# Kernel optimization log

Hardware: AMD Instinct MI355X
Metric: run time of the kernel (lower is better)

The kernel has to match this reference:

```python
import jax, jax.numpy as jnp
import numpy as np

H = 16  # head_num


def setup_inputs() -> dict:
    key = jax.random.key(0)
    ks = jax.random.split(key, 16)
    B, N, D, DR = 4, 512, 1024, 128
    dk = D // H
    nrm = lambda i, shp, sc=1.0: jax.random.normal(ks[i], shp, jnp.float32) * sc
    inp = {
        "q": nrm(0, (B, N, D)),
        "k": nrm(1, (B, N, D)),
        "v": nrm(2, (B, N, D)),
        "r_k": nrm(3, (B, N, N, DR), 0.1),
        "r_v": nrm(4, (B, N, N, DR), 0.1),
        # learned params (Linear stored as [in, out] so y = x @ W + b)
        "Wq": nrm(5, (D, D), 1.0 / np.sqrt(D)), "bq": jnp.zeros((D,), jnp.float32),
        "Wk": nrm(6, (D, D), 1.0 / np.sqrt(D)), "bk": jnp.zeros((D,), jnp.float32),
        "Wv": nrm(7, (D, D), 1.0 / np.sqrt(D)), "bv": jnp.zeros((D,), jnp.float32),
        "Wrk": nrm(8, (DR, dk), 1.0 / np.sqrt(DR)), "brk": jnp.zeros((dk,), jnp.float32),
        "Wrv": nrm(9, (DR, dk), 1.0 / np.sqrt(DR)), "brv": jnp.zeros((dk,), jnp.float32),
        "Wo": nrm(10, (D, D), 1.0 / np.sqrt(D)), "bo": jnp.zeros((D,), jnp.float32),
    }
    return inp


def reference(q, k, v, r_k, r_v, Wq, bq, Wk, bk, Wv, bv, Wrk, brk, Wrv, brv, Wo, bo):
    B, N, D = q.shape
    dk = D // H
    scale = 1.0 / np.sqrt(dk).astype(np.float32)
    # relation projections ('concat' mode, rel_share=False): [B,N,N,d_rel] -> [B,N,N,d_k]
    rk = r_k @ Wrk + brk
    rv = r_v @ Wrv + brv

    def heads(x, W, b):  # [B,N,D] -> [B,H,N,dk]
        return (x @ W + b).reshape(B, N, H, dk).transpose(0, 2, 1, 3)

    qh = heads(q, Wq, bq)
    kh = heads(k, Wk, bk)
    vh = heads(v, Wv, bv)
    # score_1: standard scaled dot-product; score_2: relation bias per (query m, key n)
    score = jnp.einsum('bhmd,bhnd->bhmn', qh, kh) * scale \
          + jnp.einsum('bhmd,bmnd->bhmn', qh, rk)
    att = jax.nn.softmax(score, axis=-1)  # [B,H,N,N]
    # value_1: standard AV; value_2: relation-value combination
    val = jnp.einsum('bhmn,bhnd->bhmd', att, vh) \
        + jnp.einsum('bhmn,bmnd->bhmd', att, rv)
    out = val.transpose(0, 2, 1, 3).reshape(B, N, D) @ Wo + bo
    return out
```

## Files before the change

kernel.cpp:

```cpp
#include <hip/hip_runtime.h>
#include <hip/hip_bf16.h>
#include <hip/hip_fp16.h>
#include <stdint.h>


typedef __attribute__((ext_vector_type(4))) float f32x4;
typedef __attribute__((ext_vector_type(8))) short s16x8;

#define MFMA16(A, B, C) __builtin_amdgcn_mfma_f32_16x16x32_bf16(A, B, C, 0, 0, 0)

__device__ __forceinline__ uint16_t f2bf(float x) {
  uint32_t u = __float_as_uint(x);
  u += 0x7fffu + ((u >> 16) & 1u);
  return (uint16_t)(u >> 16);
}
__device__ __forceinline__ float bf2f(uint16_t u) {
  return __uint_as_float((uint32_t)u << 16);
}
__device__ __forceinline__ uint16_t f2h(float x) {
  __half h = __float2half_rn(x);
  return *reinterpret_cast<uint16_t*>(&h);
}
__device__ __forceinline__ float h2f(uint16_t u) {
  __half h = *reinterpret_cast<__half*>(&u);
  return __half2float(h);
}

__device__ __forceinline__ uint32_t cvtpk(float lo, float hi) {
  uint32_t r;
  asm("v_cvt_pk_bf16_f32 %0, %1, %2" : "=v"(r) : "v"(lo), "v"(hi));
  return r;
}

__device__ __forceinline__ s16x8 pack8(float4 a, float4 b) {
  union { uint32_t u[4]; s16x8 v; } r;
  r.u[0] = cvtpk(a.x, a.y);
  r.u[1] = cvtpk(a.z, a.w);
  r.u[2] = cvtpk(b.x, b.y);
  r.u[3] = cvtpk(b.z, b.w);
  return r.v;
}

__device__ __forceinline__ void gll16(const void* g, void* l) {
  __builtin_amdgcn_global_load_lds(
      (const __attribute__((address_space(1))) uint32_t*)(g),
      (__attribute__((address_space(3))) uint32_t*)(l), 16, 0, 0);
}

__global__ __launch_bounds__(256) void k_prep(
    const float* __restrict__ Wq, const float* __restrict__ Wk,
    const float* __restrict__ Wv, const float* __restrict__ Wo,
    const float* __restrict__ Wrk, const float* __restrict__ Wrv,
    uint16_t* __restrict__ WqT, uint16_t* __restrict__ WkT,
    uint16_t* __restrict__ WvT, uint16_t* __restrict__ WoT,
    uint16_t* __restrict__ WrkB, uint16_t* __restrict__ WrvT) {
  int z = blockIdx.y;
  int t = threadIdx.x;
  if (z == 4) {
    if (blockIdx.x == 0) {
      for (int i = t; i < 128 * 64; i += 256) WrkB[i] = f2bf(Wrk[i]);
      for (int i = t; i < 64 * 128; i += 256) {
        int d = i >> 7, r = i & 127;
        WrvT[i] = f2bf(Wrv[r * 64 + d]);
      }
    }
    return;
  }
  const float* W = (z == 0) ? Wq : (z == 1) ? Wk : (z == 2) ? Wv : Wo;
  uint16_t* O = (z == 0) ? WqT : (z == 1) ? WkT : (z == 2) ? WvT : WoT;
  int tk = (blockIdx.x >> 4) * 64;
  int tn = (blockIdx.x & 15) * 64;
  __shared__ float tile[64][65];
  {
    int kk = t >> 2, c0 = (t & 3) * 16;
    const float* src = W + (size_t)(tk + kk) * 1024 + tn + c0;
#pragma unroll
    for (int i = 0; i < 16; i += 4) {
      float4 v = *(const float4*)(src + i);
      tile[kk][c0 + i + 0] = v.x; tile[kk][c0 + i + 1] = v.y;
      tile[kk][c0 + i + 2] = v.z; tile[kk][c0 + i + 3] = v.w;
    }
  }
  __syncthreads();
  {
    int n_loc = t >> 2;
    int n = tn + n_loc;
#pragma unroll
    for (int cc = 0; cc < 2; ++cc) {
      int c = (t & 3) * 2 + cc;
      int csrc = c ^ (n & 7);
      s16x8 pk;
#pragma unroll
      for (int j = 0; j < 8; ++j) pk[j] = (short)f2bf(tile[csrc * 8 + j][n_loc]);
      *reinterpret_cast<s16x8*>(O + (size_t)n * 1024 + tk + c * 8) = pk;
    }
  }
}

__global__ __launch_bounds__(256) void k_projqkv(
    const float* __restrict__ Xq, const float* __restrict__ Xk,
    const float* __restrict__ Xv, const uint16_t* __restrict__ WTbase,
    const float* __restrict__ bq, const float* __restrict__ bk,
    const float* __restrict__ bv, uint16_t* __restrict__ outbase) {
  int mode = blockIdx.z;
  const float* X = (mode == 0) ? Xq : (mode == 1) ? Xk : Xv;
  const float* bias = (mode == 0) ? bq : (mode == 1) ? bk : bv;
  const uint16_t* WT = WTbase + (size_t)mode * (1u << 20);
  uint16_t* out = outbase + (size_t)mode * (2u << 20);

  __shared__ alignas(16) float Xs[128 * 64];
  __shared__ alignas(16) uint16_t Bs[128 * 64];
  int t = threadIdx.x, lane = t & 63, w = t >> 6, lr = lane & 15, lg = lane >> 4;
  int m0 = blockIdx.x * 128, n0 = blockIdx.y * 128;
  int wm = (w >> 1) * 64, wn = (w & 1) * 64;
  f32x4 acc[4][4];
#pragma unroll
  for (int i = 0; i < 4; ++i)
#pragma unroll
    for (int j = 0; j < 4; ++j) acc[i][j] = (f32x4){0.f, 0.f, 0.f, 0.f};
  for (int ko = 0; ko < 16; ++ko) {
    __syncthreads();
    {
#pragma unroll
      for (int i = 0; i < 8; ++i) {
        int u = i * 256 + t;
        int row = u >> 4, c16 = u & 15;
        int cs = c16 ^ (row & 15);
        gll16(X + (size_t)(m0 + row) * 1024 + ko * 64 + cs * 4, (char*)Xs + u * 16);
      }
#pragma unroll
      for (int i = 0; i < 4; ++i) {
        int u = i * 256 + t;
        int row = u >> 3, c2 = u & 7;
        gll16(WT + (size_t)(n0 + row) * 1024 + ko * 64 + c2 * 8, (char*)Bs + u * 16);
      }
    }
    __syncthreads();
#pragma unroll
    for (int kk = 0; kk < 2; ++kk) {
      s16x8 af[4], bf[4];
#pragma unroll
      for (int mt = 0; mt < 4; ++mt) {
        int row = wm + mt * 16 + lr;
        int c0 = kk * 8 + lg * 2;
        float4 v0 = *(const float4*)((const char*)Xs + row * 256 +
                                     ((c0 ^ (row & 15)) * 16));
        float4 v1 = *(const float4*)((const char*)Xs + row * 256 +
                                     (((c0 + 1) ^ (row & 15)) * 16));
        af[mt] = pack8(v0, v1);
      }
#pragma unroll
      for (int nt = 0; nt < 4; ++nt) {
        int row = wn + nt * 16 + lr;
        bf[nt] = *(const s16x8*)((const char*)Bs + row * 128 +
                                 (((kk * 32 + lg * 8) * 2) ^ ((row & 7) << 4)));
      }
#pragma unroll
      for (int mt = 0; mt < 4; ++mt)
#pragma unroll
        for (int nt = 0; nt < 4; ++nt)
          acc[mt][nt] = MFMA16(af[mt], bf[nt], acc[mt][nt]);
    }
  }
  float sc = (mode == 1) ? 0.125f : 1.0f;
#pragma unroll
  for (int mt = 0; mt < 4; ++mt) {
#pragma unroll
    for (int nt = 0; nt < 4; ++nt) {
      int col = n0 + wn + nt * 16 + lr;
      float bcol = bias[col];
      if (mode != 2) {
#pragma unroll
        for (int r = 0; r < 4; ++r) {
          int row = m0 + wm + mt * 16 + lg * 4 + r;
          out[(size_t)row * 1024 + col] = f2bf((acc[mt][nt][r] + bcol) * sc);
        }
      } else {
        int row0 = m0 + wm + mt * 16 + lg * 4;
        int b = row0 >> 9, n = row0 & 511;
        int h = col >> 6, d = col & 63;
        ushort4 pk;
        pk.x = f2bf(acc[mt][nt][0] + bcol);
        pk.y = f2bf(acc[mt][nt][1] + bcol);
        pk.z = f2bf(acc[mt][nt][2] + bcol);
        pk.w = f2bf(acc[mt][nt][3] + bcol);
        *reinterpret_cast<ushort4*>(out + ((size_t)(b * 16 + h) * 64 + d) * 512 + n) = pk;
      }
    }
  }
}

__global__ __launch_bounds__(256) void k_score1qt(
    const uint16_t* __restrict__ qh, const uint16_t* __restrict__ kh,
    const uint16_t* __restrict__ WrkB, uint16_t* __restrict__ S1,
    uint16_t* __restrict__ qt) {
  __shared__ alignas(16) uint16_t As[128 * 64];
  __shared__ alignas(16) uint16_t Bs[128 * 64];
  int t = threadIdx.x, lane = t & 63, w = t >> 6, lr = lane & 15, lg = lane >> 4;
  int b = blockIdx.z;
  if (blockIdx.y >= 16) {
    int slot = (blockIdx.y - 16) * 64 + b * 16 + blockIdx.x;
#pragma unroll
    for (int it = 0; it < 2; ++it) {
      int row0 = slot * 128 + it * 64 + w * 16;
      f32x4 acc[8];
#pragma unroll
      for (int i = 0; i < 8; ++i) acc[i] = (f32x4){0.f, 0.f, 0.f, 0.f};
      s16x8 af[2];
#pragma unroll
      for (int kk = 0; kk < 2; ++kk)
        af[kk] = *(const s16x8*)(qh + (size_t)(row0 + lr) * 64 + kk * 32 + lg * 8);
#pragma unroll
      for (int rt = 0; rt < 8; ++rt) {
#pragma unroll
        for (int kk = 0; kk < 2; ++kk) {
          s16x8 bf = *(const s16x8*)(WrkB + (size_t)(rt * 16 + lr) * 64 + kk * 32 + lg * 8);
          acc[rt] = MFMA16(af[kk], bf, acc[rt]);
        }
      }
#pragma unroll
      for (int rt = 0; rt < 8; ++rt)
#pragma unroll
        for (int r = 0; r < 4; ++r)
          qt[(size_t)(row0 + lg * 4 + r) * 128 + rt * 16 + lr] = f2bf(acc[rt][r]);
    }
    return;
  }
  int mt = blockIdx.x >> 2, nt = blockIdx.x & 3, h = blockIdx.y;
  int m0 = mt * 128, n0 = nt * 128;
  const char* qg = (const char*)(qh + (size_t)(b * 512 + m0) * 1024 + h * 64);
  const char* kg = (const char*)(kh + (size_t)(b * 512 + n0) * 1024 + h * 64);
#pragma unroll
  for (int i = 0; i < 4; ++i) {
    int u = i * 256 + t;
    int row = u >> 3;
    int cs = (u & 7) ^ (row & 7);
    gll16(qg + (size_t)row * 2048 + cs * 16, (char*)As + u * 16);
    gll16(kg + (size_t)row * 2048 + cs * 16, (char*)Bs + u * 16);
  }
  __syncthreads();
  int wm = (w >> 1) * 64, wn = (w & 1) * 64;
  f32x4 acc[4][4];
#pragma unroll
  for (int i = 0; i < 4; ++i)
#pragma unroll
    for (int j = 0; j < 4; ++j) acc[i][j] = (f32x4){0.f, 0.f, 0.f, 0.f};
#pragma unroll
  for (int kk = 0; kk < 2; ++kk) {
    s16x8 af[4], bf[4];
#pragma unroll
    for (int mtt = 0; mtt < 4; ++mtt) {
      int row = wm + mtt * 16 + lr;
      af[mtt] = *(const s16x8*)((const char*)As + row * 128 +
                                (((kk * 4 + lg) ^ (row & 7)) * 16));
    }
#pragma unroll
    for (int ntt = 0; ntt < 4; ++ntt) {
      int row = wn + ntt * 16 + lr;
      bf[ntt] = *(const s16x8*)((const char*)Bs + row * 128 +
                                (((kk * 4 + lg) ^ (row & 7)) * 16));
    }
#pragma unroll
    for (int mtt = 0; mtt < 4; ++mtt)
#pragma unroll
      for (int ntt = 0; ntt < 4; ++ntt)
        acc[mtt][ntt] = MFMA16(bf[ntt], af[mtt], acc[mtt][ntt]);
  }
  int hsw = (h & 7) << 3;
#pragma unroll
  for (int mtt = 0; mtt < 4; ++mtt) {
#pragma unroll
    for (int ntt = 0; ntt < 4; ++ntt) {
      int m = b * 512 + m0 + wm + mtt * 16 + lr;
      int nsw = (n0 + wn + ntt * 16 + lg * 4) ^ hsw;
      ushort4 u4;
      u4.x = f2h(acc[mtt][ntt][0]); u4.y = f2h(acc[mtt][ntt][1]);
      u4.z = f2h(acc[mtt][ntt][2]); u4.w = f2h(acc[mtt][ntt][3]);
      *(ushort4*)(S1 + (size_t)m * 8192 + h * 512 + nsw) = u4;
    }
  }
}

#define RKSTEP(s)                                                              \
  {                                                                            \
    asm volatile("s_waitcnt vmcnt(%0)" ::                                      \
                 "i"(((s) < 2) ? 6 : (((s) < 31) ? 2 : 0)) : "memory");        \
    const char* bp_ = wpriv + ((s) & 1) * 2048 + lr * 128;                     \
    float4 v0_ = *(const float4*)(bp_ + (((lg * 2 + 0) ^ (lr & 7)) * 16));     \
    float4 v1_ = *(const float4*)(bp_ + (((lg * 2 + 1) ^ (lr & 7)) * 16));     \
    acc[(s) >> 2] = MFMA16(aqt[(s) & 3], pack8(v0_, v1_), acc[(s) >> 2]);      \
    if ((s) + 2 < 32) {                                                        \
      const int s2_ = (s) + 2;                                                 \
      const char* src_ = rkb + (size_t)((s2_ >> 2) * 64 + w * 16 + r_lo) * 512 \
                         + (s2_ & 3) * 128 + c16s * 16;                        \
      char* dst_ = wpriv + (s2_ & 1) * 2048 + lane * 16;                       \
      gll16(src_, dst_);                                                       \
      gll16(src_ + 8 * 512, dst_ + 1024);                                      \
    }                                                                          \
  }

#define RVI(c)                                                                 \
  { _Pragma("unroll")                                                          \
    for (int i_ = 0; i_ < 2; ++i_) {                                           \
      int u_ = i_ * 64 + lane;                                                 \
      gll16(rvb + (size_t)(((c) >> 1) * 32 + (u_ >> 2)) * 512 + w * 128 +      \
                ((c) & 1) * 64 + (u_ & 3) * 16,                                \
            wpriv + ((c) & 1) * 2048 + u_ * 16);                               \
    } }

#define RVC(c, accv)                                                           \
  {                                                                            \
    s16x8 a_ = *(const s16x8*)((const char*)att_lds + lr * 1024 +              \
        (((uint32_t)(((c) >> 1) * 64 + lg * 16)) ^ ((uint32_t)(lr & 7) << 4)));\
    const float* vb_ = (const float*)(wpriv + ((c) & 1) * 2048);               \
    union { uint32_t u[4]; s16x8 v; } bb_;                                     \
    _Pragma("unroll")                                                          \
    for (int i = 0; i < 4; ++i)                                                \
      bb_.u[i] = cvtpk(vb_[(lg * 8 + 2 * i) * 16 + lr],                        \
                       vb_[(lg * 8 + 2 * i + 1) * 16 + lr]);                   \
    accv = MFMA16(a_, bb_.v, accv);                                            \
  }

__global__ __launch_bounds__(256, 4) void k_s2v2(
    const uint16_t* __restrict__ qt, const float* __restrict__ rk,
    const float* __restrict__ rv, uint16_t* SATT,
    const uint16_t* __restrict__ WrvT, const float* __restrict__ brv,
    uint16_t* __restrict__ V2) {
  int bm = blockIdx.x;
  int t = threadIdx.x, lane = t & 63, w = t >> 6, lr = lane & 15, lg = lane >> 4;
  __shared__ alignas(16) char stream_lds[16384];
  __shared__ alignas(16) uint16_t att_lds[16 * 512];
  __shared__ alignas(16) uint16_t arv_lds[16 * 128];
  __shared__ float red[2][16][4];
  char* wpriv = stream_lds + w * 4096;
  const int r_lo = lane >> 3;
  const int c16s = (lane & 7) ^ r_lo;

  s16x8 aqt[4];
#pragma unroll
  for (int kk = 0; kk < 4; ++kk)
    aqt[kk] = *(const s16x8*)(qt + ((size_t)bm * 16 + lr) * 128 + kk * 32 + lg * 8);

  const char* rkb = (const char*)(rk + (size_t)bm * 65536);
#pragma unroll
  for (int s2 = 0; s2 < 2; ++s2) {
    const char* src_ = rkb + (size_t)(w * 16 + r_lo) * 512 + s2 * 128 + c16s * 16;
    char* dst_ = wpriv + s2 * 2048 + lane * 16;
    gll16(src_, dst_);
    gll16(src_ + 8 * 512, dst_ + 1024);
  }
  const char* s1g = (const char*)(SATT + (size_t)bm * 8192);
#pragma unroll
  for (int i = 0; i < 4; ++i)
    gll16(s1g + i * 4096 + t * 16, (char*)att_lds + i * 4096 + t * 16);

  f32x4 acc[8];
#pragma unroll
  for (int j = 0; j < 8; ++j) acc[j] = (f32x4){0.f, 0.f, 0.f, 0.f};

  RKSTEP(0)  RKSTEP(1)  RKSTEP(2)  RKSTEP(3)  RKSTEP(4)  RKSTEP(5)  RKSTEP(6)  RKSTEP(7)
  RKSTEP(8)  RKSTEP(9)  RKSTEP(10) RKSTEP(11) RKSTEP(12) RKSTEP(13) RKSTEP(14) RKSTEP(15)
  RKSTEP(16) RKSTEP(17) RKSTEP(18) RKSTEP(19) RKSTEP(20) RKSTEP(21) RKSTEP(22) RKSTEP(23)
  RKSTEP(24) RKSTEP(25) RKSTEP(26) RKSTEP(27) RKSTEP(28) RKSTEP(29) RKSTEP(30) RKSTEP(31)

  __syncthreads();

  const char* rvb = (const char*)(rv + (size_t)bm * 65536);
  RVI(0) RVI(1)

#pragma unroll
  for (int idx = 0; idx < 8; ++idx) {
#pragma unroll
    for (int r = 0; r < 4; ++r) {
      int h = lg * 4 + r;
      int n = idx * 64 + w * 16 + lr;
      uint16_t s1v = *(const uint16_t*)((const char*)att_lds + h * 1024 +
                     (((uint32_t)n * 2) ^ ((uint32_t)(h & 7) << 4)));
      acc[idx][r] += h2f(s1v);
    }
  }

  float mrow[4], inv[4];
#pragma unroll
  for (int r = 0; r < 4; ++r) {
    float mx = acc[0][r];
#pragma unroll
    for (int j = 1; j < 8; ++j) mx = fmaxf(mx, acc[j][r]);
#pragma unroll
    for (int off = 1; off < 16; off <<= 1) mx = fmaxf(mx, __shfl_xor(mx, off, 64));
    mrow[r] = mx;
  }
  if (lr == 0) {
#pragma unroll
    for (int r = 0; r < 4; ++r) red[0][lg * 4 + r][w] = mrow[r];
  }
  __syncthreads();
#pragma unroll
  for (int r = 0; r < 4; ++r) {
    const float* p = red[0][lg * 4 + r];
    mrow[r] = fmaxf(fmaxf(p[0], p[1]), fmaxf(p[2], p[3]));
  }
#pragma unroll
  for (int r = 0; r < 4; ++r) {
    float s = 0.f;
#pragma unroll
    for (int j = 0; j < 8; ++j) {
      float pj = __expf(acc[j][r] - mrow[r]);
      acc[j][r] = pj;
      s += pj;
    }
#pragma unroll
    for (int off = 1; off < 16; off <<= 1) s += __shfl_xor(s, off, 64);
    inv[r] = s;
  }
  if (lr == 0) {
#pragma unroll
    for (int r = 0; r < 4; ++r) red[1][lg * 4 + r][w] = inv[r];
  }
  __syncthreads();
#pragma unroll
  for (int r = 0; r < 4; ++r) {
    const float* p = red[1][lg * 4 + r];
    inv[r] = 1.f / (p[0] + p[1] + p[2] + p[3]);
  }
#pragma unroll
  for (int r = 0; r < 4; ++r) {
    int h = lg * 4 + r;
#pragma unroll
    for (int idx = 0; idx < 8; ++idx) {
      int n = idx * 64 + w * 16 + lr;
      uint32_t off = (uint32_t)h * 1024 + (((uint32_t)n * 2) ^ ((uint32_t)(h & 7) << 4));
      *(uint16_t*)((char*)att_lds + off) = f2bf(acc[idx][r] * inv[r]);
    }
  }
  __syncthreads();

  f32x4 arv0 = (f32x4){0.f, 0.f, 0.f, 0.f}, arv1 = arv0;
#pragma unroll 1
  for (int cp = 0; cp < 14; ++cp) {
    asm volatile("s_waitcnt vmcnt(2)" ::: "memory");
    RVC(2 * cp, arv0)
    RVI(2 * cp + 2)
    asm volatile("s_waitcnt vmcnt(2)" ::: "memory");
    RVC(2 * cp + 1, arv1)
    RVI(2 * cp + 3)
  }
  asm volatile("s_waitcnt vmcnt(2)" ::: "memory");
  RVC(28, arv0)
  RVI(30)
  asm volatile("s_waitcnt vmcnt(2)" ::: "memory");
  RVC(29, arv1)
  RVI(31)
  asm volatile("s_waitcnt vmcnt(2)" ::: "memory");
  RVC(30, arv0)
  asm volatile("s_waitcnt vmcnt(0)" ::: "memory");
  RVC(31, arv1)

#pragma unroll
  for (int r = 0; r < 4; ++r) {
    int h = lg * 4 + r;
    uint32_t rc0 = (uint32_t)(w * 32 + lr) * 2;
    uint32_t rc1 = (uint32_t)(w * 32 + 16 + lr) * 2;
    *(uint16_t*)((char*)arv_lds + h * 256 + (rc0 ^ ((uint32_t)(h & 7) << 4))) = f2bf(arv0[r]);
    *(uint16_t*)((char*)arv_lds + h * 256 + (rc1 ^ ((uint32_t)(h & 7) << 4))) = f2bf(arv1[r]);
  }
  __syncthreads();
  f32x4 vacc = (f32x4){0.f, 0.f, 0.f, 0.f};
#pragma unroll
  for (int kk = 0; kk < 4; ++kk) {
    uint32_t rb = (uint32_t)(kk * 32 + lg * 8) * 2;
    s16x8 a = *(const s16x8*)((const char*)arv_lds + lr * 256 +
                              (rb ^ ((uint32_t)(lr & 7) << 4)));
    s16x8 bfw = *(const s16x8*)(WrvT + (size_t)(w * 16 + lr) * 128 + kk * 32 + lg * 8);
    vacc = MFMA16(a, bfw, vacc);
  }
  float bias = brv[w * 16 + lr];
#pragma unroll
  for (int r = 0; r < 4; ++r)
    V2[(size_t)bm * 1024 + (lg * 4 + r) * 64 + w * 16 + lr] = f2bf(vacc[r] + bias);

#pragma unroll
  for (int i = 0; i < 4; ++i) {
    s16x8 vv = *(const s16x8*)((const char*)att_lds + i * 4096 + t * 16);
    *(s16x8*)((char*)SATT + (size_t)bm * 16384 + i * 4096 + t * 16) = vv;
  }
}

__global__ __launch_bounds__(256, 4) void k_val1(
    const uint16_t* __restrict__ vhT, const uint16_t* __restrict__ ATT,
    const uint16_t* __restrict__ V2, uint16_t* __restrict__ VALB) {
  int t = threadIdx.x, lane = t & 63, w = t >> 6, lr = lane & 15, lg = lane >> 4;
  int mt = blockIdx.x >> 1, dh = blockIdx.x & 1, h = blockIdx.y, b = blockIdx.z;
  int mb = mt * 64 + w * 16;
  const uint16_t* vrow = vhT + ((size_t)((b * 16 + h) * 64) + dh * 32 + lr) * 512 + lg * 8;
  const uint16_t* arow = ATT + (size_t)(b * 512 + mb + lr) * 8192 + h * 512;
  f32x4 acc[2];
#pragma unroll
  for (int j = 0; j < 2; ++j) acc[j] = (f32x4){0.f, 0.f, 0.f, 0.f};
#pragma unroll
  for (int kk = 0; kk < 16; ++kk) {
    int nsw = (kk * 32 + lg * 8) ^ ((h & 7) << 3);
    s16x8 a0 = *(const s16x8*)(arow + nsw);
#pragma unroll
    for (int dt = 0; dt < 2; ++dt) {
      s16x8 vf = *(const s16x8*)(vrow + (size_t)dt * 16 * 512 + kk * 32);
      acc[dt] = MFMA16(vf, a0, acc[dt]);
    }
  }
#pragma unroll
  for (int dt = 0; dt < 2; ++dt) {
    size_t adr = (size_t)(b * 512 + mb + lr) * 1024 + h * 64 + dh * 32 + dt * 16 + lg * 4;
    ushort4 v2v = *(const ushort4*)(V2 + adr);
    ushort4 o;
    o.x = f2bf(acc[dt][0] + bf2f(v2v.x));
    o.y = f2bf(acc[dt][1] + bf2f(v2v.y));
    o.z = f2bf(acc[dt][2] + bf2f(v2v.z));
    o.w = f2bf(acc[dt][3] + bf2f(v2v.w));
    *(ushort4*)(VALB + adr) = o;
  }
}

__global__ __launch_bounds__(256) void k_out(
    const uint16_t* __restrict__ A, const uint16_t* __restrict__ WT,
    const float* __restrict__ bias, float* __restrict__ out) {
  __shared__ alignas(16) uint16_t As[128 * 64];
  __shared__ alignas(16) uint16_t Bs[128 * 64];
  int t = threadIdx.x, lane = t & 63, w = t >> 6, lr = lane & 15, lg = lane >> 4;
  int m0 = blockIdx.x * 128, n0 = blockIdx.y * 128;
  int wm = (w >> 1) * 64, wn = (w & 1) * 64;
  f32x4 acc[4][4];
#pragma unroll
  for (int i = 0; i < 4; ++i)
#pragma unroll
    for (int j = 0; j < 4; ++j) acc[i][j] = (f32x4){0.f, 0.f, 0.f, 0.f};
  for (int ko = 0; ko < 16; ++ko) {
    __syncthreads();
    {
#pragma unroll
      for (int i = 0; i < 4; ++i) {
        int u = i * 256 + t;
        int row = u >> 3, c2 = u & 7;
        int cs = c2 ^ (row & 7);
        gll16(A + (size_t)(m0 + row) * 1024 + ko * 64 + cs * 8, (char*)As + u * 16);
        gll16(WT + (size_t)(n0 + row) * 1024 + ko * 64 + c2 * 8, (char*)Bs + u * 16);
      }
    }
    __syncthreads();
#pragma unroll
    for (int kk = 0; kk < 2; ++kk) {
      s16x8 af[4], bf[4];
#pragma unroll
      for (int mt = 0; mt < 4; ++mt) {
        int row = wm + mt * 16 + lr;
        af[mt] = *(const s16x8*)((const char*)As + row * 128 +
                                 (((kk * 32 + lg * 8) * 2) ^ ((row & 7) << 4)));
      }
#pragma unroll
      for (int nt = 0; nt < 4; ++nt) {
        int row = wn + nt * 16 + lr;
        bf[nt] = *(const s16x8*)((const char*)Bs + row * 128 +
                                 (((kk * 32 + lg * 8) * 2) ^ ((row & 7) << 4)));
      }
#pragma unroll
      for (int mt = 0; mt < 4; ++mt)
#pragma unroll
        for (int nt = 0; nt < 4; ++nt)
          acc[mt][nt] = MFMA16(af[mt], bf[nt], acc[mt][nt]);
    }
  }
#pragma unroll
  for (int mt = 0; mt < 4; ++mt) {
#pragma unroll
    for (int nt = 0; nt < 4; ++nt) {
      int col = n0 + wn + nt * 16 + lr;
      float bcol = bias[col];
#pragma unroll
      for (int r = 0; r < 4; ++r) {
        int row = m0 + wm + mt * 16 + lg * 4 + r;
        out[(size_t)row * 1024 + col] = acc[mt][nt][r] + bcol;
      }
    }
  }
}

extern "C" void kernel_launch(void* const* d_in, const int* in_sizes, int n_in,
                              void* d_out, int out_size, void* d_ws, size_t ws_size,
                              hipStream_t stream) {
  const float* q   = (const float*)d_in[0];
  const float* k_  = (const float*)d_in[1];
  const float* v   = (const float*)d_in[2];
  const float* r_k = (const float*)d_in[3];
  const float* r_v = (const float*)d_in[4];
  const float* Wq  = (const float*)d_in[5];
  const float* bq  = (const float*)d_in[6];
  const float* Wk  = (const float*)d_in[7];
  const float* bk  = (const float*)d_in[8];
  const float* Wv  = (const float*)d_in[9];
  const float* bv  = (const float*)d_in[10];
  const float* Wrk = (const float*)d_in[11];
  const float* Wrv = (const float*)d_in[13];
  const float* brv = (const float*)d_in[14];
  const float* Wo  = (const float*)d_in[15];
  const float* bo  = (const float*)d_in[16];
  (void)in_sizes; (void)n_in; (void)out_size;

  char* ws = (char*)d_ws;
  uint16_t* WqT  = (uint16_t*)(ws + (size_t)(0));
  uint16_t* WkT  = (uint16_t*)(ws + (size_t)(2u << 20));
  uint16_t* WvT  = (uint16_t*)(ws + (size_t)(4u << 20));
  uint16_t* WoT  = (uint16_t*)(ws + (size_t)(6u << 20));
  uint16_t* WrkB = (uint16_t*)(ws + (size_t)(8u << 20));
  uint16_t* WrvT = (uint16_t*)(ws + (size_t)(8u << 20) + (64u << 10));
  uint16_t* QH   = (uint16_t*)(ws + (size_t)(16u << 20));
  uint16_t* KH   = (uint16_t*)(ws + (size_t)(20u << 20));
  uint16_t* VHT  = (uint16_t*)(ws + (size_t)(24u << 20));
  uint16_t* QT   = (uint16_t*)(ws + (size_t)(28u << 20));
  uint16_t* VALB = (uint16_t*)(ws + (size_t)(36u << 20));
  uint16_t* V2   = (uint16_t*)(ws + (size_t)(16u << 20));
  uint16_t* SATT = (uint16_t*)(ws + (size_t)(40u << 20));
  if (ws_size < (size_t)(74u << 20)) return;

  dim3 blk(256, 1, 1);
  k_prep<<<dim3(256, 5, 1), blk, 0, stream>>>(Wq, Wk, Wv, Wo, Wrk, Wrv,
                                              WqT, WkT, WvT, WoT, WrkB, WrvT);
  k_projqkv<<<dim3(16, 8, 3), blk, 0, stream>>>(q, k_, v, WqT, bq, bk, bv, QH);
  k_score1qt<<<dim3(16, 20, 4), blk, 0, stream>>>(QH, KH, WrkB, SATT, QT);
  k_s2v2<<<dim3(2048, 1, 1), blk, 0, stream>>>(QT, r_k, r_v, SATT, WrvT, brv, V2);
  k_val1<<<dim3(16, 16, 4), blk, 0, stream>>>(VHT, SATT, V2, VALB);
  k_out<<<dim3(16, 8, 1), blk, 0, stream>>>(VALB, WoT, bo, (float*)d_out);
}
```

Before: 344.9 us.

## Reuse Q tile across key tiles with double-buffered K in score kernel

The score1 kernel now has each block keep one Q tile in shared memory and loop over all four key tiles, double-buffering the K tiles through async loads so the next tile's fetch overlaps the current MFMA work. The qt-projection blocks each handle twice as many rows, and the grid shrinks from 1280 to 384 blocks. k_val1 now computes all 64 head dims per block instead of splitting them in two, so attention rows are loaded once rather than twice. Both changes cut redundant global loads in exchange for fewer blocks, and so less parallelism and latency hiding.

Result: no change. 341.4 us (-1.0%).

```diff
diff --git a/kernel.cpp b/kernel.cpp
--- a/kernel.cpp
+++ b/kernel.cpp
@@ -194,15 +194,15 @@
     const uint16_t* __restrict__ qh, const uint16_t* __restrict__ kh,
     const uint16_t* __restrict__ WrkB, uint16_t* __restrict__ S1,
     uint16_t* __restrict__ qt) {
-  __shared__ alignas(16) uint16_t As[128 * 64];
-  __shared__ alignas(16) uint16_t Bs[128 * 64];
+  __shared__ alignas(16) uint16_t Qs[128 * 64];
+  __shared__ alignas(16) uint16_t Ks[2][128 * 64];
   int t = threadIdx.x, lane = t & 63, w = t >> 6, lr = lane & 15, lg = lane >> 4;
   int b = blockIdx.z;
-  if (blockIdx.y >= 16) {
-    int slot = (blockIdx.y - 16) * 64 + b * 16 + blockIdx.x;
-#pragma unroll
-    for (int it = 0; it < 2; ++it) {
-      int row0 = slot * 128 + it * 64 + w * 16;
+  if (blockIdx.x >= 4) {
+    int slot = (blockIdx.x - 4) * 64 + blockIdx.y * 4 + b;
+#pragma unroll
+    for (int it = 0; it < 4; ++it) {
+      int row0 = slot * 256 + it * 64 + w * 16;
       f32x4 acc[8];
 #pragma unroll
       for (int i = 0; i < 8; ++i) acc[i] = (f32x4){0.f, 0.f, 0.f, 0.f};
@@ -226,57 +226,72 @@
     }
     return;
   }
-  int mt = blockIdx.x >> 2, nt = blockIdx.x & 3, h = blockIdx.y;
-  int m0 = mt * 128, n0 = nt * 128;
+  int mt = blockIdx.x, h = blockIdx.y;
+  int m0 = mt * 128;
   const char* qg = (const char*)(qh + (size_t)(b * 512 + m0) * 1024 + h * 64);
-  const char* kg = (const char*)(kh + (size_t)(b * 512 + n0) * 1024 + h * 64);
+  const char* kg = (const char*)(kh + (size_t)b * 512 * 1024 + h * 64);
 #pragma unroll
   for (int i = 0; i < 4; ++i) {
     int u = i * 256 + t;
     int row = u >> 3;
     int cs = (u & 7) ^ (row & 7);
-    gll16(qg + (size_t)row * 2048 + cs * 16, (char*)As + u * 16);
-    gll16(kg + (size_t)row * 2048 + cs * 16, (char*)Bs + u * 16);
-  }
-  __syncthreads();
+    gll16(qg + (size_t)row * 2048 + cs * 16, (char*)Qs + u * 16);
+    gll16(kg + (size_t)row * 2048 + cs * 16, (char*)Ks[0] + u * 16);
+  }
   int wm = (w >> 1) * 64, wn = (w & 1) * 64;
-  f32x4 acc[4][4];
-#pragma unroll
-  for (int i = 0; i < 4; ++i)
-#pragma unroll
-    for (int j = 0; j < 4; ++j) acc[i][j] = (f32x4){0.f, 0.f, 0.f, 0.f};
-#pragma unroll
-  for (int kk = 0; kk < 2; ++kk) {
-    s16x8 af[4], bf[4];
+  int hsw = (h & 7) << 3;
+#pragma unroll
+  for (int nt = 0; nt < 4; ++nt) {
+    asm volatile("s_waitcnt vmcnt(0)" ::: "memory");
+    __builtin_amdgcn_s_barrier();
+    asm volatile("" ::: "memory");
+    if (nt < 3) {
+      const char* kgn = kg + (size_t)(nt + 1) * 128 * 2048;
+#pragma unroll
+      for (int i = 0; i < 4; ++i) {
+        int u = i * 256 + t;
+        int row = u >> 3;
+        int cs = (u & 7) ^ (row & 7);
+        gll16(kgn + (size_t)row * 2048 + cs * 16, (char*)Ks[(nt + 1) & 1] + u * 16);
+      }
+    }
+    f32x4 acc[4][4];
+#pragma unroll
+    for (int i = 0; i < 4; ++i)
+#pragma unroll
+      for (int j = 0; j < 4; ++j) acc[i][j] = (f32x4){0.f, 0.f, 0.f, 0.f};
+#pragma unroll
+    for (int kk = 0; kk < 2; ++kk) {
+      s16x8 af[4], bf[4];
+#pragma unroll
+      for (int mtt = 0; mtt < 4; ++mtt) {
+        int row = wm + mtt * 16 + lr;
+        af[mtt] = *(const s16x8*)((const char*)Qs + row * 128 +
+                                  (((kk * 4 + lg) ^ (row & 7)) * 16));
+      }
+#pragma unroll
+      for (int ntt = 0; ntt < 4; ++ntt) {
+        int row = wn + ntt * 16 + lr;
+        bf[ntt] = *(const s16x8*)((const char*)Ks[nt & 1] + row * 128 +
+                                  (((kk * 4 + lg) ^ (row & 7)) * 16));
+      }
+#pragma unroll
+      for (int mtt = 0; mtt < 4; ++mtt)
+#pragma unroll
+        for (int ntt = 0; ntt < 4; ++ntt)
+          acc[mtt][ntt] = MFMA16(bf[ntt], af[mtt], acc[mtt][ntt]);
+    }
 #pragma unroll
     for (int mtt = 0; mtt < 4; ++mtt) {
-      int row = wm + mtt * 16 + lr;
-      af[mtt] = *(const s16x8*)((const char*)As + row * 128 +
-                                (((kk * 4 + lg) ^ (row & 7)) * 16));
-    }
-#pragma unroll
-    for (int ntt = 0; ntt < 4; ++ntt) {
-      int row = wn + ntt * 16 + lr;
-      bf[ntt] = *(const s16x8*)((const char*)Bs + row * 128 +
-                                (((kk * 4 + lg) ^ (row & 7)) * 16));
-    }
-#pragma unroll
-    for (int mtt = 0; mtt < 4; ++mtt)
-#pragma unroll
-      for (int ntt = 0; ntt < 4; ++ntt)
-        acc[mtt][ntt] = MFMA16(bf[ntt], af[mtt], acc[mtt][ntt]);
-  }
-  int hsw = (h & 7) << 3;
-#pragma unroll
-  for (int mtt = 0; mtt < 4; ++mtt) {
-#pragma unroll
-    for (int ntt = 0; ntt < 4; ++ntt) {
-      int m = b * 512 + m0 + wm + mtt * 16 + lr;
-      int nsw = (n0 + wn + ntt * 16 + lg * 4) ^ hsw;
-      ushort4 u4;
-      u4.x = f2h(acc[mtt][ntt][0]); u4.y = f2h(acc[mtt][ntt][1]);
-      u4.z = f2h(acc[mtt][ntt][2]); u4.w = f2h(acc[mtt][ntt][3]);
-      *(ushort4*)(S1 + (size_t)m * 8192 + h * 512 + nsw) = u4;
+#pragma unroll
+      for (int ntt = 0; ntt < 4; ++ntt) {
+        int m = b * 512 + m0 + wm + mtt * 16 + lr;
+        int nsw = (nt * 128 + wn + ntt * 16 + lg * 4) ^ hsw;
+        ushort4 u4;
+        u4.x = f2h(acc[mtt][ntt][0]); u4.y = f2h(acc[mtt][ntt][1]);
+        u4.z = f2h(acc[mtt][ntt][2]); u4.w = f2h(acc[mtt][ntt][3]);
+        *(ushort4*)(S1 + (size_t)m * 8192 + h * 512 + nsw) = u4;
+      }
     }
   }
 }
@@ -490,26 +505,26 @@
     const uint16_t* __restrict__ vhT, const uint16_t* __restrict__ ATT,
     const uint16_t* __restrict__ V2, uint16_t* __restrict__ VALB) {
   int t = threadIdx.x, lane = t & 63, w = t >> 6, lr = lane & 15, lg = lane >> 4;
-  int mt = blockIdx.x >> 1, dh = blockIdx.x & 1, h = blockIdx.y, b = blockIdx.z;
+  int mt = blockIdx.x, h = blockIdx.y, b = blockIdx.z;
   int mb = mt * 64 + w * 16;
-  const uint16_t* vrow = vhT + ((size_t)((b * 16 + h) * 64) + dh * 32 + lr) * 512 + lg * 8;
+  const uint16_t* vrow = vhT + ((size_t)((b * 16 + h) * 64) + lr) * 512 + lg * 8;
   const uint16_t* arow = ATT + (size_t)(b * 512 + mb + lr) * 8192 + h * 512;
-  f32x4 acc[2];
-#pragma unroll
-  for (int j = 0; j < 2; ++j) acc[j] = (f32x4){0.f, 0.f, 0.f, 0.f};
-#pragma unroll
+  f32x4 acc[4];
+#pragma unroll
+  for (int j = 0; j < 4; ++j) acc[j] = (f32x4){0.f, 0.f, 0.f, 0.f};
+#pragma unroll 4
   for (int kk = 0; kk < 16; ++kk) {
     int nsw = (kk * 32 + lg * 8) ^ ((h & 7) << 3);
     s16x8 a0 = *(const s16x8*)(arow + nsw);
 #pragma unroll
-    for (int dt = 0; dt < 2; ++dt) {
+    for (int dt = 0; dt < 4; ++dt) {
       s16x8 vf = *(const s16x8*)(vrow + (size_t)dt * 16 * 512 + kk * 32);
       acc[dt] = MFMA16(vf, a0, acc[dt]);
     }
   }
 #pragma unroll
-  for (int dt = 0; dt < 2; ++dt) {
-    size_t adr = (size_t)(b * 512 + mb + lr) * 1024 + h * 64 + dh * 32 + dt * 16 + lg * 4;
+  for (int dt = 0; dt < 4; ++dt) {
+    size_t adr = (size_t)(b * 512 + mb + lr) * 1024 + h * 64 + dt * 16 + lg * 4;
     ushort4 v2v = *(const ushort4*)(V2 + adr);
     ushort4 o;
     o.x = f2bf(acc[dt][0] + bf2f(v2v.x));
@@ -624,8 +639,8 @@
   k_prep<<<dim3(256, 5, 1), blk, 0, stream>>>(Wq, Wk, Wv, Wo, Wrk, Wrv,
                                               WqT, WkT, WvT, WoT, WrkB, WrvT);
   k_projqkv<<<dim3(16, 8, 3), blk, 0, stream>>>(q, k_, v, WqT, bq, bk, bv, QH);
-  k_score1qt<<<dim3(16, 20, 4), blk, 0, stream>>>(QH, KH, WrkB, SATT, QT);
+  k_score1qt<<<dim3(6, 16, 4), blk, 0, stream>>>(QH, KH, WrkB, SATT, QT);
   k_s2v2<<<dim3(2048, 1, 1), blk, 0, stream>>>(QT, r_k, r_v, SATT, WrvT, brv, V2);
-  k_val1<<<dim3(16, 16, 4), blk, 0, stream>>>(VHT, SATT, V2, VALB);
+  k_val1<<<dim3(8, 16, 4), blk, 0, stream>>>(VHT, SATT, V2, VALB);
   k_out<<<dim3(16, 8, 1), blk, 0, stream>>>(VALB, WoT, bo, (float*)d_out);
 }
```
